# Kernel tuning notes

Measured on AMD Instinct MI355X. Metric: run time of the kernel, lower is better.

## Reference

```python
import jax, jax.numpy as jnp
import numpy as np

N_ATOMS = 10000
N_PAIR = 100000
F = 128
N_HEAD = 4
FH = F // N_HEAD  # 32
DEGREES = [1, 2, 3]
N_DEG = len(DEGREES)
REPEATS = np.array([2 * l + 1 for l in DEGREES])  # [3,5,7]
M_TOT = int(REPEATS.sum())  # 15
K_RBF = 32


def ssp(x):
    # shifted softplus: softplus(x) - log(2)
    return jax.nn.softplus(x) - jnp.log(2.0).astype(x.dtype)


def setup_inputs() -> dict:
    key = jax.random.key(0)
    ks = jax.random.split(key, 16)
    inp = {
        "x": jax.random.normal(ks[0], (N_ATOMS, F), jnp.float32),
        "rbf_ij": jax.random.normal(ks[1], (N_PAIR, K_RBF), jnp.float32),
        "sph_ij": jax.random.normal(ks[2], (N_PAIR, M_TOT), jnp.float32),
        "phi_r_cut": jax.random.uniform(ks[3], (N_PAIR,), jnp.float32),
        "idx_i": jnp.sort(jax.random.randint(ks[4], (N_PAIR,), 0, N_ATOMS)),
        "idx_j": jax.random.randint(ks[5], (N_PAIR,), 0, N_ATOMS),
        "pair_mask": jnp.ones((N_PAIR,), jnp.float32),
        # params
        "W_Q": jax.random.normal(ks[6], (N_DEG, N_HEAD, FH, FH), jnp.float32) / np.sqrt(FH),
        "W_K": jax.random.normal(ks[7], (N_DEG, N_HEAD, FH, FH), jnp.float32) / np.sqrt(FH),
        # in2f MLP: single dense F -> F
        "W_in": jax.random.normal(ks[8], (F, F), jnp.float32) / np.sqrt(F),
        "b_in": jnp.zeros((F,), jnp.float32),
        # radial filter MLP: K -> K (ssp) -> n_deg*F
        "W_f1": jax.random.normal(ks[9], (K_RBF, K_RBF), jnp.float32) / np.sqrt(K_RBF),
        "b_f1": jnp.zeros((K_RBF,), jnp.float32),
        "W_f2": jax.random.normal(ks[10], (K_RBF, N_DEG * F), jnp.float32) / np.sqrt(K_RBF),
        "b_f2": jnp.zeros((N_DEG * F,), jnp.float32),
        # f2out MLP: single dense F -> F
        "W_out": jax.random.normal(ks[11], (F, F), jnp.float32) / np.sqrt(F),
        "b_out": jnp.zeros((F,), jnp.float32),
    }
    return inp


def reference(x, rbf_ij, sph_ij, phi_r_cut, idx_i, idx_j, pair_mask,
              W_Q, W_K, W_in, b_in, W_f1, b_f1, W_f2, b_f2, W_out, b_out):
    n = x.shape[0]
    # in2f embedding (last in2f dim == F)
    x_f = x @ W_in + b_in                                  # (n, F)
    x_head = x_f.reshape(n, N_HEAD, FH)                    # (n, h, FH)

    # per-degree, per-head linear maps (the nested vmap matmuls)
    Q = jnp.einsum('dhij,nhj->ndhi', W_Q, x_head)          # (n, n_deg, h, FH)
    K = jnp.einsum('dhij,nhj->ndhi', W_K, x_head)

    m = pair_mask[:, None, None, None]
    Q_i = Q[idx_i] * m                                     # (P, n_deg, h, FH)
    K_j = K[idx_j] * m

    # radial filter: MLP(rbf) -> (P, n_deg, h, FH), scaled by cutoff
    h1 = ssp(rbf_ij @ W_f1 + b_f1)
    W_ij = (h1 @ W_f2 + b_f2).reshape(-1, N_DEG, N_HEAD, FH)
    W_ij = W_ij * phi_r_cut[:, None, None, None]

    # attention coefficients per degree/head
    alpha = jnp.sum(Q_i * K_j * W_ij, axis=-1)             # (P, n_deg, h)
    alpha = jnp.repeat(alpha, repeats=REPEATS, axis=1, total_repeat_length=M_TOT)  # (P, m_tot, h)
    alpha = alpha / jnp.sqrt(jnp.asarray(FH, x.dtype))     # att_scale

    # outer product of neighbor features with spherical harmonics
    x_j = x_head[idx_j] * pair_mask[:, None, None]         # (P, h, FH)
    z_ij = jnp.einsum('pm,phf->pmhf', sph_ij, x_j)         # (P, m_tot, h, FH)
    z_ij = alpha[:, :, :, None] * z_ij
    z_ij = z_ij.reshape(z_ij.shape[0], M_TOT, F)           # (P, m_tot, F)

    agg = jax.ops.segment_sum(z_ij, idx_i, num_segments=n)  # (n, m_tot, F)

    # f2out projection (last f2out dim == F)
    out = agg @ W_out + b_out                               # (n, m_tot, F)
    return out
```

## Files before the change

kernel.cpp:

```cpp
#include <hip/hip_runtime.h>
#include <hip/hip_bf16.h>

#define N_ATOMS 10000
#define N_PAIR  100000
#define F_DIM   128
#define N_HEAD  4
#define FH      32
#define N_DEG   3
#define M_TOT   15
#define K_RBF   32
#define R_OUT   (N_ATOMS * M_TOT)

typedef __attribute__((ext_vector_type(8))) short short8;
typedef __attribute__((ext_vector_type(4))) float f32x4;

union frag_cast { int i[4]; short8 s; };

__device__ __forceinline__ float sspf(float v) {
    float sp = fmaxf(v, 0.f) + log1pf(expf(-fabsf(v)));
    return sp - 0.69314718055994531f;
}

__device__ __forceinline__ unsigned short bf16_rne(float x) {
    unsigned int u = __float_as_uint(x);
    unsigned int r = u + 0x7fffu + ((u >> 16) & 1u);
    return (unsigned short)(r >> 16);
}
__device__ __forceinline__ float bf16_tof(unsigned short h) {
    return __uint_as_float(((unsigned int)h) << 16);
}

__global__ __launch_bounds__(256) void k_gemm128(
    const float* __restrict__ A, const float* __restrict__ B,
    const float* __restrict__ bias, float* __restrict__ C, int rows)
{
    __shared__ float As[32][132];
    __shared__ float Bs[32][132];
    int r0 = blockIdx.x * 128;
    int t = threadIdx.x;
    int ty = t >> 4, tx = t & 15;

    float acc[8][8];
    #pragma unroll
    for (int i = 0; i < 8; ++i)
        #pragma unroll
        for (int j = 0; j < 8; ++j) acc[i][j] = 0.f;

    for (int k0 = 0; k0 < 128; k0 += 32) {
        #pragma unroll
        for (int r = 0; r < 16; ++r) {
            int idx = t + 256 * r;
            int row = idx >> 5, kk = idx & 31;
            int grow = r0 + row;
            As[kk][row] = (grow < rows) ? A[grow * 128 + k0 + kk] : 0.f;
        }
        #pragma unroll
        for (int r = 0; r < 16; ++r) {
            int idx = t + 256 * r;
            int kk = idx >> 7, c = idx & 127;
            Bs[kk][c] = B[(k0 + kk) * 128 + c];
        }
        __syncthreads();

        #pragma unroll
        for (int kk = 0; kk < 32; ++kk) {
            float a[8], b[8];
            *(float4*)&a[0] = *(const float4*)&As[kk][ty * 4];
            *(float4*)&a[4] = *(const float4*)&As[kk][64 + ty * 4];
            *(float4*)&b[0] = *(const float4*)&Bs[kk][tx * 4];
            *(float4*)&b[4] = *(const float4*)&Bs[kk][64 + tx * 4];
            #pragma unroll
            for (int i = 0; i < 8; ++i)
                #pragma unroll
                for (int j = 0; j < 8; ++j)
                    acc[i][j] = fmaf(a[i], b[j], acc[i][j]);
        }
        __syncthreads();
    }

    float bj[8];
    #pragma unroll
    for (int j = 0; j < 4; ++j) { bj[j] = bias[tx * 4 + j]; bj[4 + j] = bias[64 + tx * 4 + j]; }

    #pragma unroll
    for (int i = 0; i < 8; ++i) {
        int row = r0 + ((i < 4) ? (ty * 4 + i) : (64 + ty * 4 + (i - 4)));
        if (row < rows) {
            float4 v0, v1;
            v0.x = acc[i][0] + bj[0]; v0.y = acc[i][1] + bj[1];
            v0.z = acc[i][2] + bj[2]; v0.w = acc[i][3] + bj[3];
            v1.x = acc[i][4] + bj[4]; v1.y = acc[i][5] + bj[5];
            v1.z = acc[i][6] + bj[6]; v1.w = acc[i][7] + bj[7];
            *(float4*)&C[row * 128 + tx * 4] = v0;
            *(float4*)&C[row * 128 + 64 + tx * 4] = v1;
        }
    }
}

__global__ __launch_bounds__(384) void k_qk(
    const float* __restrict__ xh, const float* __restrict__ W_Q,
    const float* __restrict__ W_K, float* __restrict__ Q, float* __restrict__ K)
{
    __shared__ float xfs[32][128];
    int t = threadIdx.x;
    int h = (t >> 5) & 3;
    float wq[32], wk[32];
    const float4* wqp = (const float4*)(W_Q + t * 32);
    const float4* wkp = (const float4*)(W_K + t * 32);
    #pragma unroll
    for (int j4 = 0; j4 < 8; ++j4) {
        float4 a = wqp[j4], b = wkp[j4];
        wq[4 * j4 + 0] = a.x; wq[4 * j4 + 1] = a.y; wq[4 * j4 + 2] = a.z; wq[4 * j4 + 3] = a.w;
        wk[4 * j4 + 0] = b.x; wk[4 * j4 + 1] = b.y; wk[4 * j4 + 2] = b.z; wk[4 * j4 + 3] = b.w;
    }
    int ab = blockIdx.x * 32;
    for (int idx = t; idx < 4096; idx += 384) {
        int aa = idx >> 7, f = idx & 127;
        int ag = ab + aa;
        xfs[aa][f] = (ag < N_ATOMS) ? xh[ag * 128 + f] : 0.f;
    }
    __syncthreads();
    for (int aa = 0; aa < 32; ++aa) {
        int ag = ab + aa;
        if (ag >= N_ATOMS) break;
        const float4* xv = (const float4*)&xfs[aa][h * 32];
        float q0 = 0.f, q1 = 0.f, k0 = 0.f, k1 = 0.f;
        #pragma unroll
        for (int j4 = 0; j4 < 8; j4 += 2) {
            float4 x0 = xv[j4], x1 = xv[j4 + 1];
            q0 = fmaf(wq[4 * j4 + 0], x0.x, q0); q0 = fmaf(wq[4 * j4 + 1], x0.y, q0);
            q0 = fmaf(wq[4 * j4 + 2], x0.z, q0); q0 = fmaf(wq[4 * j4 + 3], x0.w, q0);
            q1 = fmaf(wq[4 * j4 + 4], x1.x, q1); q1 = fmaf(wq[4 * j4 + 5], x1.y, q1);
            q1 = fmaf(wq[4 * j4 + 6], x1.z, q1); q1 = fmaf(wq[4 * j4 + 7], x1.w, q1);
            k0 = fmaf(wk[4 * j4 + 0], x0.x, k0); k0 = fmaf(wk[4 * j4 + 1], x0.y, k0);
            k0 = fmaf(wk[4 * j4 + 2], x0.z, k0); k0 = fmaf(wk[4 * j4 + 3], x0.w, k0);
            k1 = fmaf(wk[4 * j4 + 4], x1.x, k1); k1 = fmaf(wk[4 * j4 + 5], x1.y, k1);
            k1 = fmaf(wk[4 * j4 + 6], x1.z, k1); k1 = fmaf(wk[4 * j4 + 7], x1.w, k1);
        }
        Q[ag * 384 + t] = q0 + q1;
        K[ag * 384 + t] = k0 + k1;
    }
}

__global__ __launch_bounds__(384) void k_pair(
    const float* __restrict__ rbf, const float* __restrict__ phi,
    const float* __restrict__ mask, const int* __restrict__ idx_i,
    const int* __restrict__ idx_j, const float* __restrict__ W_f1,
    const float* __restrict__ b_f1, const float* __restrict__ W_f2,
    const float* __restrict__ b_f2, const float* __restrict__ Q,
    const float* __restrict__ K, float* __restrict__ alpha)
{
    __shared__ float wf1s[32][33];
    __shared__ float b1s[32];
    __shared__ float rbf_s[64][36];
    __shared__ float h1_s[64][36];
    __shared__ float phi_s[64];
    __shared__ float m_s[64];
    __shared__ int   i_s[64];
    __shared__ int   j_s[64];
    __shared__ float alpha_s[64 * 12];

    int t = threadIdx.x;
    int p0 = blockIdx.x * 64;
    int pr = t / 192;
    int c  = t % 192;
    int dh = c >> 4;
    int f0 = c & 15;
    int e0 = dh * 32 + f0;
    int e1 = e0 + 16;

    float wf2a[32], wf2b[32];
    #pragma unroll
    for (int k = 0; k < 32; ++k) {
        wf2a[k] = W_f2[k * 384 + e0];
        wf2b[k] = W_f2[k * 384 + e1];
    }
    float b2a = b_f2[e0], b2b = b_f2[e1];

    for (int idx = t; idx < 1024; idx += 384) wf1s[idx >> 5][idx & 31] = W_f1[idx];
    if (t < 32) b1s[t] = b_f1[t];
    for (int idx = t; idx < 2048; idx += 384) {
        int pp = idx >> 5, l = idx & 31;
        int pg = p0 + pp;
        rbf_s[pp][l] = (pg < N_PAIR) ? rbf[pg * 32 + l] : 0.f;
    }
    if (t < 64) {
        int pg = p0 + t;
        bool v = pg < N_PAIR;
        phi_s[t] = v ? phi[pg] : 0.f;
        m_s[t]   = v ? mask[pg] : 0.f;
        i_s[t]   = v ? idx_i[pg] : 0;
        j_s[t]   = v ? idx_j[pg] : 0;
    }
    __syncthreads();

    for (int idx = t; idx < 2048; idx += 384) {
        int pp = idx >> 5, l = idx & 31;
        float acc = b1s[l];
        #pragma unroll
        for (int k = 0; k < 32; ++k)
            acc = fmaf(rbf_s[pp][k], wf1s[k][l], acc);
        h1_s[pp][l] = sspf(acc);
    }
    __syncthreads();

    float qa0 = Q[i_s[pr] * 384 + e0],     qb0 = Q[i_s[pr] * 384 + e1];
    float ka0 = K[j_s[pr] * 384 + e0],     kb0 = K[j_s[pr] * 384 + e1];
    float qa1 = Q[i_s[pr + 2] * 384 + e0], qb1 = Q[i_s[pr + 2] * 384 + e1];
    float ka1 = K[j_s[pr + 2] * 384 + e0], kb1 = K[j_s[pr + 2] * 384 + e1];

    for (int pb = 0; pb < 64; pb += 4) {
        int pA = pb + pr, pB = pb + 2 + pr;
        float nqa0, nqb0, nka0, nkb0, nqa1, nqb1, nka1, nkb1;
        if (pb < 60) {
            int nA = pA + 4, nB = pB + 4;
            nqa0 = Q[i_s[nA] * 384 + e0]; nqb0 = Q[i_s[nA] * 384 + e1];
            nka0 = K[j_s[nA] * 384 + e0]; nkb0 = K[j_s[nA] * 384 + e1];
            nqa1 = Q[i_s[nB] * 384 + e0]; nqb1 = Q[i_s[nB] * 384 + e1];
            nka1 = K[j_s[nB] * 384 + e0]; nkb1 = K[j_s[nB] * 384 + e1];
        }
        float w00 = b2a, w01 = b2b, w10 = b2a, w11 = b2b;
        #pragma unroll
        for (int k4 = 0; k4 < 8; ++k4) {
            float4 h0 = *(const float4*)&h1_s[pA][k4 * 4];
            float4 h1v = *(const float4*)&h1_s[pB][k4 * 4];
            w00 = fmaf(h0.x, wf2a[4 * k4 + 0], w00); w00 = fmaf(h0.y, wf2a[4 * k4 + 1], w00);
            w00 = fmaf(h0.z, wf2a[4 * k4 + 2], w00); w00 = fmaf(h0.w, wf2a[4 * k4 + 3], w00);
            w01 = fmaf(h0.x, wf2b[4 * k4 + 0], w01); w01 = fmaf(h0.y, wf2b[4 * k4 + 1], w01);
            w01 = fmaf(h0.z, wf2b[4 * k4 + 2], w01); w01 = fmaf(h0.w, wf2b[4 * k4 + 3], w01);
            w10 = fmaf(h1v.x, wf2a[4 * k4 + 0], w10); w10 = fmaf(h1v.y, wf2a[4 * k4 + 1], w10);
            w10 = fmaf(h1v.z, wf2a[4 * k4 + 2], w10); w10 = fmaf(h1v.w, wf2a[4 * k4 + 3], w10);
            w11 = fmaf(h1v.x, wf2b[4 * k4 + 0], w11); w11 = fmaf(h1v.y, wf2b[4 * k4 + 1], w11);
            w11 = fmaf(h1v.z, wf2b[4 * k4 + 2], w11); w11 = fmaf(h1v.w, wf2b[4 * k4 + 3], w11);
        }
        float part0 = (qa0 * ka0 * w00 + qb0 * kb0 * w01) * phi_s[pA];
        float part1 = (qa1 * ka1 * w10 + qb1 * kb1 * w11) * phi_s[pB];
        #pragma unroll
        for (int off = 8; off >= 1; off >>= 1) {
            part0 += __shfl_xor(part0, off, 16);
            part1 += __shfl_xor(part1, off, 16);
        }
        if (f0 == 0) {
            float m0 = m_s[pA], m1 = m_s[pB];
            alpha_s[pA * 12 + dh] = part0 * m0 * m0 * 0.17677669529663687f;
            alpha_s[pB * 12 + dh] = part1 * m1 * m1 * 0.17677669529663687f;
        }
        if (pb < 60) {
            qa0 = nqa0; qb0 = nqb0; ka0 = nka0; kb0 = nkb0;
            qa1 = nqa1; qb1 = nqb1; ka1 = nka1; kb1 = nkb1;
        }
    }
    __syncthreads();
    #pragma unroll
    for (int r = 0; r < 2; ++r) {
        int idx = t + r * 384;
        int g = p0 * 12 + idx;
        if (g < N_PAIR * 12) alpha[g] = alpha_s[idx];
    }
}

__device__ __forceinline__ int lower_bound_i(const int* __restrict__ arr, int n, int val) {
    int lo = 0, hi = n;
    while (lo < hi) {
        int mid = (lo + hi) >> 1;
        if (arr[mid] < val) lo = mid + 1; else hi = mid;
    }
    return lo;
}

__global__ __launch_bounds__(256) void k_seg(const int* __restrict__ idx_i,
                                             int* __restrict__ seg)
{
    int a = blockIdx.x * 256 + threadIdx.x;
    if (a <= N_ATOMS) seg[a] = lower_bound_i(idx_i, N_PAIR, a);
}

__global__ __launch_bounds__(256) void k_cvt_b(
    const float* __restrict__ W, unsigned short* __restrict__ Bth,
    unsigned short* __restrict__ Btl)
{
    int idx = blockIdx.x * 256 + threadIdx.x;
    int cc = idx >> 7, kk = idx & 127;
    float v = W[kk * 128 + cc];
    unsigned short h = bf16_rne(v);
    unsigned short l = bf16_rne(v - bf16_tof(h));
    Bth[cc * 128 + kk] = h;
    Btl[cc * 128 + kk] = l;
}

__global__ __launch_bounds__(256) void k_agg(
    const float* __restrict__ xh, const float* __restrict__ alpha,
    const float* __restrict__ sph, const int* __restrict__ seg,
    const int* __restrict__ idx_j, const float* __restrict__ mask,
    unsigned int* __restrict__ aggp)
{
    __shared__ float red[15][132];
    int a = blockIdx.x;
    int t = threadIdx.x & 127;
    int grp = threadIdx.x >> 7;
    int h = t >> 5;
    int lo = seg[a], hi = seg[a + 1];

    float acc[15];
    #pragma unroll
    for (int m = 0; m < 15; ++m) acc[m] = 0.f;

    int p = lo + grp;
    float x_cur = 0.f;
    if (p < hi) x_cur = xh[idx_j[p] * 128 + t];
    for (; p < hi; p += 2) {
        int pn = p + 2;
        float x_nxt = 0.f;
        if (pn < hi) x_nxt = xh[idx_j[pn] * 128 + t];
        float xj = x_cur * mask[p];
        float a0v = alpha[p * 12 + h];
        float a1v = alpha[p * 12 + 4 + h];
        float a2v = alpha[p * 12 + 8 + h];
        const float* sp = sph + p * 15;
        #pragma unroll
        for (int m = 0; m < 15; ++m) {
            float al = (m < 3) ? a0v : ((m < 8) ? a1v : a2v);
            acc[m] = fmaf(sp[m] * al, xj, acc[m]);
        }
        x_cur = x_nxt;
    }

    if (grp == 1) {
        #pragma unroll
        for (int m = 0; m < 15; ++m) red[m][t] = acc[m];
    }
    __syncthreads();
    if (grp == 0) {
        #pragma unroll
        for (int m = 0; m < 15; ++m) {
            float v = acc[m] + red[m][t];
            unsigned short hh = bf16_rne(v);
            unsigned short ll = bf16_rne(v - bf16_tof(hh));
            aggp[(a * 15 + m) * 128 + t] = ((unsigned int)hh << 16) | (unsigned int)ll;
        }
    }
}

__global__ __launch_bounds__(256) void k_out_mfma(
    const unsigned int* __restrict__ Apack,
    const unsigned short* __restrict__ Bth, const unsigned short* __restrict__ Btl,
    const float* __restrict__ bias, float* __restrict__ C)
{
    int t = threadIdx.x;
    int wave = t >> 6, lane = t & 63;
    int quad = lane >> 4, l15 = lane & 15;
    long rowbase = (long)blockIdx.x * 128 + wave * 32;

    short8 ah[2][4], al[2][4];
    #pragma unroll
    for (int rt = 0; rt < 2; ++rt) {
        long row = rowbase + rt * 16 + l15;
        if (row > R_OUT - 1) row = R_OUT - 1;
        #pragma unroll
        for (int ks = 0; ks < 4; ++ks) {
            const uint4* ap = (const uint4*)(Apack + row * 128 + ks * 32 + quad * 8);
            uint4 u01 = ap[0], u23 = ap[1];
            unsigned int u[8] = {u01.x, u01.y, u01.z, u01.w, u23.x, u23.y, u23.z, u23.w};
            frag_cast fh, fl;
            #pragma unroll
            for (int q = 0; q < 4; ++q) {
                unsigned int a0 = u[2 * q], a1 = u[2 * q + 1];
                fh.i[q] = (int)((a0 >> 16) | (a1 & 0xffff0000u));
                fl.i[q] = (int)((a0 & 0xffffu) | (a1 << 16));
            }
            ah[rt][ks] = fh.s;
            al[rt][ks] = fl.s;
        }
    }

    #pragma unroll 2
    for (int nt = 0; nt < 8; ++nt) {
        int colbase = nt * 16;
        short8 bh[4], bl[4];
        #pragma unroll
        for (int ks = 0; ks < 4; ++ks) {
            int off = (colbase + l15) * 128 + ks * 32 + quad * 8;
            bh[ks] = *(const short8*)(Bth + off);
            bl[ks] = *(const short8*)(Btl + off);
        }
        f32x4 acc0 = {0.f, 0.f, 0.f, 0.f};
        f32x4 acc1 = {0.f, 0.f, 0.f, 0.f};
        #pragma unroll
        for (int ks = 0; ks < 4; ++ks) {
            acc0 = __builtin_amdgcn_mfma_f32_16x16x32_bf16(ah[0][ks], bh[ks], acc0, 0, 0, 0);
            acc1 = __builtin_amdgcn_mfma_f32_16x16x32_bf16(ah[1][ks], bh[ks], acc1, 0, 0, 0);
            acc0 = __builtin_amdgcn_mfma_f32_16x16x32_bf16(al[0][ks], bh[ks], acc0, 0, 0, 0);
            acc1 = __builtin_amdgcn_mfma_f32_16x16x32_bf16(al[1][ks], bh[ks], acc1, 0, 0, 0);
            acc0 = __builtin_amdgcn_mfma_f32_16x16x32_bf16(ah[0][ks], bl[ks], acc0, 0, 0, 0);
            acc1 = __builtin_amdgcn_mfma_f32_16x16x32_bf16(ah[1][ks], bl[ks], acc1, 0, 0, 0);
        }
        float bv = bias[colbase + l15];
        #pragma unroll
        for (int r = 0; r < 4; ++r) {
            long row0 = rowbase + quad * 4 + r;
            long row1 = rowbase + 16 + quad * 4 + r;
            if (row0 < R_OUT) C[row0 * 128 + colbase + l15] = acc0[r] + bv;
            if (row1 < R_OUT) C[row1 * 128 + colbase + l15] = acc1[r] + bv;
        }
    }
}

extern "C" void kernel_launch(void* const* d_in, const int* in_sizes, int n_in,
                              void* d_out, int out_size, void* d_ws, size_t ws_size,
                              hipStream_t stream) {
    const float* x        = (const float*)d_in[0];
    const float* rbf_ij   = (const float*)d_in[1];
    const float* sph_ij   = (const float*)d_in[2];
    const float* phi_r    = (const float*)d_in[3];
    const int*   idx_i    = (const int*)d_in[4];
    const int*   idx_j    = (const int*)d_in[5];
    const float* pmask    = (const float*)d_in[6];
    const float* W_Q      = (const float*)d_in[7];
    const float* W_K      = (const float*)d_in[8];
    const float* W_in     = (const float*)d_in[9];
    const float* b_in     = (const float*)d_in[10];
    const float* W_f1     = (const float*)d_in[11];
    const float* b_f1     = (const float*)d_in[12];
    const float* W_f2     = (const float*)d_in[13];
    const float* b_f2     = (const float*)d_in[14];
    const float* W_out    = (const float*)d_in[15];
    const float* b_out    = (const float*)d_in[16];
    float* out = (float*)d_out;

    float* ws    = (float*)d_ws;
    float* xh    = ws;
    float* Qbuf  = xh + N_ATOMS * F_DIM;
    float* Kbuf  = Qbuf + N_ATOMS * 384;
    float* alpha = Kbuf + N_ATOMS * 384;
    int*   seg   = (int*)(alpha + N_PAIR * 12);
    unsigned short* Bth = (unsigned short*)(seg + 10432);
    unsigned short* Btl = Bth + 16384;

    k_seg<<<(N_ATOMS + 256) / 256, 256, 0, stream>>>(idx_i, seg);
    k_cvt_b<<<64, 256, 0, stream>>>(W_out, Bth, Btl);
    k_gemm128<<<(N_ATOMS + 127) / 128, 256, 0, stream>>>(x, W_in, b_in, xh, N_ATOMS);
    k_qk<<<(N_ATOMS + 31) / 32, 384, 0, stream>>>(xh, W_Q, W_K, Qbuf, Kbuf);
    k_pair<<<(N_PAIR + 63) / 64, 384, 0, stream>>>(rbf_ij, phi_r, pmask, idx_i, idx_j,
                                                   W_f1, b_f1, W_f2, b_f2, Qbuf, Kbuf, alpha);
    k_agg<<<N_ATOMS, 256, 0, stream>>>(xh, alpha, sph_ij, seg, idx_j, pmask,
                                       (unsigned int*)d_out);
    k_out_mfma<<<(R_OUT + 127) / 128, 256, 0, stream>>>((const unsigned int*)d_out,
                                                        Bth, Btl, b_out, out);
}
```

Before: 393.1 us.

## Compute pair radial filter with split-bf16 MFMA and coalesced Q*K gather

```diff
diff --git a/kernel.cpp b/kernel.cpp
--- a/kernel.cpp
+++ b/kernel.cpp
@@ -142,120 +142,155 @@
     }
 }
 
-__global__ __launch_bounds__(384) void k_pair(
+__global__ __launch_bounds__(256) void k_cvt_w2(
+    const float* __restrict__ W, unsigned short* __restrict__ Wh,
+    unsigned short* __restrict__ Wl)
+{
+    int idx = blockIdx.x * 256 + threadIdx.x;
+    if (idx < 12288) {
+        int e = idx >> 5, k = idx & 31;
+        float v = W[k * 384 + e];
+        unsigned short h = bf16_rne(v);
+        unsigned short l = bf16_rne(v - bf16_tof(h));
+        Wh[e * 32 + k] = h;
+        Wl[e * 32 + k] = l;
+    }
+}
+
+__global__ __launch_bounds__(256) void k_pair(
     const float* __restrict__ rbf, const float* __restrict__ phi,
     const float* __restrict__ mask, const int* __restrict__ idx_i,
     const int* __restrict__ idx_j, const float* __restrict__ W_f1,
-    const float* __restrict__ b_f1, const float* __restrict__ W_f2,
-    const float* __restrict__ b_f2, const float* __restrict__ Q,
-    const float* __restrict__ K, float* __restrict__ alpha)
-{
-    __shared__ float wf1s[32][33];
-    __shared__ float b1s[32];
-    __shared__ float rbf_s[64][36];
-    __shared__ float h1_s[64][36];
-    __shared__ float phi_s[64];
-    __shared__ float m_s[64];
-    __shared__ int   i_s[64];
-    __shared__ int   j_s[64];
-    __shared__ float alpha_s[64 * 12];
+    const float* __restrict__ b_f1, const unsigned short* __restrict__ W2h,
+    const unsigned short* __restrict__ W2l, const float* __restrict__ b_f2,
+    const float* __restrict__ Q, const float* __restrict__ K,
+    float* __restrict__ alpha)
+{
+    __shared__ float g_s[32][384];
+    __shared__ unsigned int h1p_s[32][36];
+    __shared__ int   i_s[32];
+    __shared__ int   j_s[32];
+    __shared__ float phim_s[32];
+
+    float (*rbf_s)[33] = (float (*)[33])(&g_s[0][0]);
+    float (*wf1_s)[33] = (float (*)[33])(&g_s[0][0] + 32 * 33);
 
     int t = threadIdx.x;
-    int p0 = blockIdx.x * 64;
-    int pr = t / 192;
-    int c  = t % 192;
-    int dh = c >> 4;
-    int f0 = c & 15;
-    int e0 = dh * 32 + f0;
-    int e1 = e0 + 16;
-
-    float wf2a[32], wf2b[32];
-    #pragma unroll
-    for (int k = 0; k < 32; ++k) {
-        wf2a[k] = W_f2[k * 384 + e0];
-        wf2b[k] = W_f2[k * 384 + e1];
-    }
-    float b2a = b_f2[e0], b2b = b_f2[e1];
-
-    for (int idx = t; idx < 1024; idx += 384) wf1s[idx >> 5][idx & 31] = W_f1[idx];
-    if (t < 32) b1s[t] = b_f1[t];
-    for (int idx = t; idx < 2048; idx += 384) {
-        int pp = idx >> 5, l = idx & 31;
-        int pg = p0 + pp;
-        rbf_s[pp][l] = (pg < N_PAIR) ? rbf[pg * 32 + l] : 0.f;
-    }
-    if (t < 64) {
+    int p0 = blockIdx.x * 32;
+
+    for (int idx = t; idx < 1024; idx += 256) {
+        int r = idx >> 5, c = idx & 31;
+        rbf_s[r][c] = rbf[p0 * 32 + idx];
+        wf1_s[r][c] = W_f1[idx];
+    }
+    if (t < 32) {
         int pg = p0 + t;
-        bool v = pg < N_PAIR;
-        phi_s[t] = v ? phi[pg] : 0.f;
-        m_s[t]   = v ? mask[pg] : 0.f;
-        i_s[t]   = v ? idx_i[pg] : 0;
-        j_s[t]   = v ? idx_j[pg] : 0;
+        i_s[t] = idx_i[pg];
+        j_s[t] = idx_j[pg];
+        float m = mask[pg];
+        phim_s[t] = phi[pg] * m * m * 0.17677669529663687f;
     }
     __syncthreads();
 
-    for (int idx = t; idx < 2048; idx += 384) {
-        int pp = idx >> 5, l = idx & 31;
-        float acc = b1s[l];
-        #pragma unroll
-        for (int k = 0; k < 32; ++k)
-            acc = fmaf(rbf_s[pp][k], wf1s[k][l], acc);
-        h1_s[pp][l] = sspf(acc);
+    {
+        int p = t >> 3, c4 = (t & 7) * 4;
+        float acc0 = b_f1[c4 + 0], acc1 = b_f1[c4 + 1];
+        float acc2 = b_f1[c4 + 2], acc3 = b_f1[c4 + 3];
+        #pragma unroll
+        for (int k = 0; k < 32; ++k) {
+            float rv = rbf_s[p][k];
+            acc0 = fmaf(rv, wf1_s[k][c4 + 0], acc0);
+            acc1 = fmaf(rv, wf1_s[k][c4 + 1], acc1);
+            acc2 = fmaf(rv, wf1_s[k][c4 + 2], acc2);
+            acc3 = fmaf(rv, wf1_s[k][c4 + 3], acc3);
+        }
+        float hv[4] = {sspf(acc0), sspf(acc1), sspf(acc2), sspf(acc3)};
+        #pragma unroll
+        for (int j = 0; j < 4; ++j) {
+            unsigned short hh = bf16_rne(hv[j]);
+            unsigned short ll = bf16_rne(hv[j] - bf16_tof(hh));
+            h1p_s[p][c4 + j] = ((unsigned int)hh << 16) | (unsigned int)ll;
+        }
     }
     __syncthreads();
 
-    float qa0 = Q[i_s[pr] * 384 + e0],     qb0 = Q[i_s[pr] * 384 + e1];
-    float ka0 = K[j_s[pr] * 384 + e0],     kb0 = K[j_s[pr] * 384 + e1];
-    float qa1 = Q[i_s[pr + 2] * 384 + e0], qb1 = Q[i_s[pr + 2] * 384 + e1];
-    float ka1 = K[j_s[pr + 2] * 384 + e0], kb1 = K[j_s[pr + 2] * 384 + e1];
-
-    for (int pb = 0; pb < 64; pb += 4) {
-        int pA = pb + pr, pB = pb + 2 + pr;
-        float nqa0, nqb0, nka0, nkb0, nqa1, nqb1, nka1, nkb1;
-        if (pb < 60) {
-            int nA = pA + 4, nB = pB + 4;
-            nqa0 = Q[i_s[nA] * 384 + e0]; nqb0 = Q[i_s[nA] * 384 + e1];
-            nka0 = K[j_s[nA] * 384 + e0]; nkb0 = K[j_s[nA] * 384 + e1];
-            nqa1 = Q[i_s[nB] * 384 + e0]; nqb1 = Q[i_s[nB] * 384 + e1];
-            nka1 = K[j_s[nB] * 384 + e0]; nkb1 = K[j_s[nB] * 384 + e1];
-        }
-        float w00 = b2a, w01 = b2b, w10 = b2a, w11 = b2b;
-        #pragma unroll
-        for (int k4 = 0; k4 < 8; ++k4) {
-            float4 h0 = *(const float4*)&h1_s[pA][k4 * 4];
-            float4 h1v = *(const float4*)&h1_s[pB][k4 * 4];
-            w00 = fmaf(h0.x, wf2a[4 * k4 + 0], w00); w00 = fmaf(h0.y, wf2a[4 * k4 + 1], w00);
-            w00 = fmaf(h0.z, wf2a[4 * k4 + 2], w00); w00 = fmaf(h0.w, wf2a[4 * k4 + 3], w00);
-            w01 = fmaf(h0.x, wf2b[4 * k4 + 0], w01); w01 = fmaf(h0.y, wf2b[4 * k4 + 1], w01);
-            w01 = fmaf(h0.z, wf2b[4 * k4 + 2], w01); w01 = fmaf(h0.w, wf2b[4 * k4 + 3], w01);
-            w10 = fmaf(h1v.x, wf2a[4 * k4 + 0], w10); w10 = fmaf(h1v.y, wf2a[4 * k4 + 1], w10);
-            w10 = fmaf(h1v.z, wf2a[4 * k4 + 2], w10); w10 = fmaf(h1v.w, wf2a[4 * k4 + 3], w10);
-            w11 = fmaf(h1v.x, wf2b[4 * k4 + 0], w11); w11 = fmaf(h1v.y, wf2b[4 * k4 + 1], w11);
-            w11 = fmaf(h1v.z, wf2b[4 * k4 + 2], w11); w11 = fmaf(h1v.w, wf2b[4 * k4 + 3], w11);
-        }
-        float part0 = (qa0 * ka0 * w00 + qb0 * kb0 * w01) * phi_s[pA];
-        float part1 = (qa1 * ka1 * w10 + qb1 * kb1 * w11) * phi_s[pB];
-        #pragma unroll
-        for (int off = 8; off >= 1; off >>= 1) {
-            part0 += __shfl_xor(part0, off, 16);
-            part1 += __shfl_xor(part1, off, 16);
-        }
-        if (f0 == 0) {
-            float m0 = m_s[pA], m1 = m_s[pB];
-            alpha_s[pA * 12 + dh] = part0 * m0 * m0 * 0.17677669529663687f;
-            alpha_s[pB * 12 + dh] = part1 * m1 * m1 * 0.17677669529663687f;
-        }
-        if (pb < 60) {
-            qa0 = nqa0; qb0 = nqb0; ka0 = nka0; kb0 = nkb0;
-            qa1 = nqa1; qb1 = nqb1; ka1 = nka1; kb1 = nkb1;
-        }
+    #pragma unroll
+    for (int it = 0; it < 12; ++it) {
+        int idx = it * 256 + t;
+        int p = idx / 96;
+        int c4 = idx - p * 96;
+        const float4* qp = (const float4*)(Q + i_s[p] * 384) + c4;
+        const float4* kp = (const float4*)(K + j_s[p] * 384) + c4;
+        float4 qv = *qp, kv = *kp;
+        float4 gv;
+        gv.x = qv.x * kv.x; gv.y = qv.y * kv.y;
+        gv.z = qv.z * kv.z; gv.w = qv.w * kv.w;
+        *(float4*)&g_s[p][c4 * 4] = gv;
     }
     __syncthreads();
-    #pragma unroll
-    for (int r = 0; r < 2; ++r) {
-        int idx = t + r * 384;
-        int g = p0 * 12 + idx;
-        if (g < N_PAIR * 12) alpha[g] = alpha_s[idx];
+
+    int wave = t >> 6, lane = t & 63;
+    int quad = lane >> 4, l15 = lane & 15;
+
+    short8 ah[2], al[2];
+    #pragma unroll
+    for (int mt = 0; mt < 2; ++mt) {
+        const unsigned int* hp = &h1p_s[mt * 16 + l15][quad * 8];
+        uint4 u01 = *(const uint4*)hp;
+        uint4 u23 = *(const uint4*)(hp + 4);
+        unsigned int u[8] = {u01.x, u01.y, u01.z, u01.w, u23.x, u23.y, u23.z, u23.w};
+        frag_cast fh, fl;
+        #pragma unroll
+        for (int q = 0; q < 4; ++q) {
+            unsigned int a0 = u[2 * q], a1 = u[2 * q + 1];
+            fh.i[q] = (int)((a0 >> 16) | (a1 & 0xffff0000u));
+            fl.i[q] = (int)((a0 & 0xffffu) | (a1 << 16));
+        }
+        ah[mt] = fh.s;
+        al[mt] = fl.s;
+    }
+
+    #pragma unroll
+    for (int dd = 0; dd < 3; ++dd) {
+        int dh = wave * 3 + dd;
+        int e_base = dh * 32;
+        short8 bh0 = *(const short8*)(W2h + (e_base + l15) * 32 + quad * 8);
+        short8 bl0 = *(const short8*)(W2l + (e_base + l15) * 32 + quad * 8);
+        short8 bh1 = *(const short8*)(W2h + (e_base + 16 + l15) * 32 + quad * 8);
+        short8 bl1 = *(const short8*)(W2l + (e_base + 16 + l15) * 32 + quad * 8);
+        float b2v0 = b_f2[e_base + l15];
+        float b2v1 = b_f2[e_base + 16 + l15];
+
+        #pragma unroll
+        for (int mt = 0; mt < 2; ++mt) {
+            f32x4 s0 = {0.f, 0.f, 0.f, 0.f};
+            f32x4 s1 = {0.f, 0.f, 0.f, 0.f};
+            s0 = __builtin_amdgcn_mfma_f32_16x16x32_bf16(ah[mt], bh0, s0, 0, 0, 0);
+            s1 = __builtin_amdgcn_mfma_f32_16x16x32_bf16(ah[mt], bh1, s1, 0, 0, 0);
+            s0 = __builtin_amdgcn_mfma_f32_16x16x32_bf16(al[mt], bh0, s0, 0, 0, 0);
+            s1 = __builtin_amdgcn_mfma_f32_16x16x32_bf16(al[mt], bh1, s1, 0, 0, 0);
+            s0 = __builtin_amdgcn_mfma_f32_16x16x32_bf16(ah[mt], bl0, s0, 0, 0, 0);
+            s1 = __builtin_amdgcn_mfma_f32_16x16x32_bf16(ah[mt], bl1, s1, 0, 0, 0);
+
+            float vsum[4];
+            #pragma unroll
+            for (int r = 0; r < 4; ++r) {
+                int prow = mt * 16 + quad * 4 + r;
+                float v = (s0[r] + b2v0) * g_s[prow][e_base + l15]
+                        + (s1[r] + b2v1) * g_s[prow][e_base + 16 + l15];
+                #pragma unroll
+                for (int off = 8; off >= 1; off >>= 1)
+                    v += __shfl_xor(v, off, 16);
+                vsum[r] = v;
+            }
+            if (l15 == 0) {
+                #pragma unroll
+                for (int r = 0; r < 4; ++r) {
+                    int prow = mt * 16 + quad * 4 + r;
+                    alpha[(p0 + prow) * 12 + dh] = vsum[r] * phim_s[prow];
+                }
+            }
+        }
     }
 }
 
@@ -435,13 +470,17 @@
     int*   seg   = (int*)(alpha + N_PAIR * 12);
     unsigned short* Bth = (unsigned short*)(seg + 10432);
     unsigned short* Btl = Bth + 16384;
+    unsigned short* W2h = Btl + 16384;
+    unsigned short* W2l = W2h + 12288;
 
     k_seg<<<(N_ATOMS + 256) / 256, 256, 0, stream>>>(idx_i, seg);
     k_cvt_b<<<64, 256, 0, stream>>>(W_out, Bth, Btl);
+    k_cvt_w2<<<48, 256, 0, stream>>>(W_f2, W2h, W2l);
     k_gemm128<<<(N_ATOMS + 127) / 128, 256, 0, stream>>>(x, W_in, b_in, xh, N_ATOMS);
     k_qk<<<(N_ATOMS + 31) / 32, 384, 0, stream>>>(xh, W_Q, W_K, Qbuf, Kbuf);
-    k_pair<<<(N_PAIR + 63) / 64, 384, 0, stream>>>(rbf_ij, phi_r, pmask, idx_i, idx_j,
-                                                   W_f1, b_f1, W_f2, b_f2, Qbuf, Kbuf, alpha);
+    k_pair<<<N_PAIR / 32, 256, 0, stream>>>(rbf_ij, phi_r, pmask, idx_i, idx_j,
+                                            W_f1, b_f1, W2h, W2l, b_f2,
+                                            Qbuf, Kbuf, alpha);
     k_agg<<<N_ATOMS, 256, 0, stream>>>(xh, alpha, sph_ij, seg, idx_j, pmask,
                                        (unsigned int*)d_out);
     k_out_mfma<<<(R_OUT + 127) / 128, 256, 0, stream>>>((const unsigned int*)d_out,
```

New measurement: 374.5 us. 1.05x faster.
